# Performance work log

Hardware: AMD Instinct MI355X
Metric: run time of the kernel (lower is better)

## Reference

```python
import jax, jax.numpy as jnp
import numpy as np

S, B_BOX, C = 7, 2, 20
LAMBDA_COORD = 5.0
LAMBDA_NOOBJ = 0.5


def _iou(b1, b2):
    # b1, b2: [..., 4] in (cx, cy, w, h) format
    area1 = b1[..., 2] * b1[..., 3]
    area2 = b2[..., 2] * b2[..., 3]
    max_left = jnp.maximum(b1[..., 0] - b1[..., 2] / 2, b2[..., 0] - b2[..., 2] / 2)
    min_right = jnp.minimum(b1[..., 0] + b1[..., 2] / 2, b2[..., 0] + b2[..., 2] / 2)
    max_top = jnp.maximum(b1[..., 1] - b1[..., 3] / 2, b2[..., 1] - b2[..., 3] / 2)
    min_bottom = jnp.minimum(b1[..., 1] + b1[..., 3] / 2, b2[..., 1] + b2[..., 3] / 2)
    iw = jnp.maximum(min_right - max_left, 0.0)
    ih = jnp.maximum(min_bottom - max_top, 0.0)
    inter = iw * ih
    union = area1 + area2 - inter
    return jnp.where(inter > 0.0, inter / union, 0.0)


def setup_inputs() -> dict:
    key = jax.random.key(0)
    k1, k2, k3 = jax.random.split(key, 3)
    batch = 16384
    shape = (batch, S, S, C + 5 * B_BOX)  # [..., 30]
    pred = jax.random.uniform(k1, shape, dtype=jnp.float32)
    target = jax.random.uniform(k2, shape, dtype=jnp.float32)
    # objectness flag must be exactly 1.0 to trigger the obj branch
    obj_flag = jax.random.bernoulli(k3, 0.3, shape[:-1]).astype(jnp.float32)
    target = target.at[..., 0].set(obj_flag)
    return {"pred": pred, "target": target}


def reference(pred, target):
    batch = pred.shape[0]
    pred = pred.reshape(-1, S, S, C + 5 * B_BOX)
    target = target.reshape(-1, S, S, C + 5 * B_BOX)

    obj = (target[..., 0] == 1.0)          # [b,S,S] bool
    obj_f = obj.astype(pred.dtype)
    noobj_f = 1.0 - obj_f

    gt = target[..., 1:5]
    box1 = pred[..., 1:5]                   # predictor 1 box
    box2 = target[..., 6:10]                # NOTE: original code uses target's 2nd box
    iou1 = jax.lax.stop_gradient(_iou(box1, gt))
    iou2 = jax.lax.stop_gradient(_iou(box2, gt))
    resp1 = iou1 > iou2                     # predictor 1 responsible (strict >)
    r1 = resp1[..., None]

    # coord losses (responsible predictor)
    pxy = jnp.where(r1, pred[..., 1:3], pred[..., 6:8])
    txy = jnp.where(r1, target[..., 1:3], target[..., 6:8])
    pwh = jnp.where(r1, pred[..., 3:5], pred[..., 8:10])
    twh = jnp.where(r1, target[..., 3:5], target[..., 8:10])
    cell_xy = jnp.sum((pxy - txy) ** 2, axis=-1)
    cell_wh = jnp.sum((jnp.sqrt(pwh) - jnp.sqrt(twh)) ** 2, axis=-1)

    # obj confidence loss: responsible conf vs its iou
    conf_resp = jnp.where(resp1, pred[..., 0], pred[..., 5])
    iou_resp = jnp.where(resp1, iou1, iou2)
    cell_obj = (conf_resp - iou_resp) ** 2

    # noobj: non-responsible conf in obj cells; both confs in empty cells
    conf_other = jnp.where(resp1, pred[..., 5], pred[..., 0])
    cell_noobj_obj = conf_other ** 2
    cell_noobj_empty = pred[..., 0] ** 2 + pred[..., 5] ** 2

    cell_class = jnp.sum((pred[..., 10:] - target[..., 10:]) ** 2, axis=-1)

    loss_coord_xy = LAMBDA_COORD * jnp.sum(obj_f * cell_xy)
    loss_coord_wh = LAMBDA_COORD * jnp.sum(obj_f * cell_wh)
    loss_obj = jnp.sum(obj_f * cell_obj)
    loss_noobj = LAMBDA_NOOBJ * (jnp.sum(obj_f * cell_noobj_obj) + jnp.sum(noobj_f * cell_noobj_empty))
    loss_class = jnp.sum(obj_f * cell_class)
    loss = loss_coord_xy + loss_coord_wh + loss_obj + loss_noobj + loss_class

    bs = jnp.asarray(batch, pred.dtype)
    return ((loss_coord_xy + loss_coord_wh) / bs,
            loss_obj / bs,
            loss_noobj / bs,
            loss_class / bs,
            loss / bs)
```

## Files before the change

### kernel.cpp

```cpp
#include <hip/hip_runtime.h>

#define NCH 30
#define F2PC 15
#define CPB 256
#define THREADS 256
#define GRID 512

__device__ __forceinline__ float iou_fn(float x1, float y1, float w1, float h1,
                                        float x2, float y2, float w2, float h2) {
    float a1 = w1 * h1, a2 = w2 * h2;
    float left  = fmaxf(x1 - w1 * 0.5f, x2 - w2 * 0.5f);
    float right = fminf(x1 + w1 * 0.5f, x2 + w2 * 0.5f);
    float top   = fmaxf(y1 - h1 * 0.5f, y2 - h2 * 0.5f);
    float bot   = fminf(y1 + h1 * 0.5f, y2 + h2 * 0.5f);
    float iw = fmaxf(right - left, 0.0f);
    float ih = fmaxf(bot - top, 0.0f);
    float inter = iw * ih;
    float uni = a1 + a2 - inter;
    return (inter > 0.0f) ? (inter / uni) : 0.0f;
}

__device__ __forceinline__ void cell_losses(const float* p, const float* t,
                                            float& coord, float& lobj,
                                            float& lnoobj, float& lclass) {
    float obj_f = (t[0] == 1.0f) ? 1.0f : 0.0f;

    float iou1 = iou_fn(p[1], p[2], p[3], p[4], t[1], t[2], t[3], t[4]);
    float iou2 = iou_fn(t[6], t[7], t[8], t[9], t[1], t[2], t[3], t[4]);
    bool r = iou1 > iou2;

    float px = r ? p[1] : p[6], py = r ? p[2] : p[7];
    float pw = r ? p[3] : p[8], ph = r ? p[4] : p[9];
    float tx = r ? t[1] : t[6], ty = r ? t[2] : t[7];
    float tw = r ? t[3] : t[8], th = r ? t[4] : t[9];

    float dx = px - tx, dy = py - ty;
    float cxy = dx * dx + dy * dy;
    float swv = sqrtf(pw) - sqrtf(tw), shv = sqrtf(ph) - sqrtf(th);
    float cwh = swv * swv + shv * shv;

    float conf_resp  = r ? p[0] : p[5];
    float iou_resp   = r ? iou1 : iou2;
    float conf_other = r ? p[5] : p[0];
    float dconf = conf_resp - iou_resp;

    coord  += obj_f * (cxy + cwh);
    lobj   += obj_f * dconf * dconf;
    lnoobj += obj_f * conf_other * conf_other
            + (1.0f - obj_f) * (p[0] * p[0] + p[5] * p[5]);

    float cls = 0.0f;
#pragma unroll
    for (int i = 10; i < NCH; i++) { float e = p[i] - t[i]; cls += e * e; }
    lclass += obj_f * cls;
}

__global__ __launch_bounds__(THREADS) void yolo_main(
        const float2* __restrict__ pred2, const float2* __restrict__ targ2,
        float4* __restrict__ partials, int nchunks_full, int n_cells) {
    __shared__ float2 sp[CPB * F2PC];
    __shared__ float2 st[CPB * F2PC];

    const int tid = threadIdx.x;
    float coord = 0.f, lobj = 0.f, lnoobj = 0.f, lclass = 0.f;

    float2 rp[F2PC], rt[F2PC];

    int c = blockIdx.x;
    bool have = c < nchunks_full;
    if (have) {
        const long long b = (long long)c * (CPB * F2PC);
#pragma unroll
        for (int k = 0; k < F2PC; k++) {
            rp[k] = pred2[b + tid + k * THREADS];
            rt[k] = targ2[b + tid + k * THREADS];
        }
    }

    while (have) {
        int cn = c + gridDim.x;
        bool have_n = cn < nchunks_full;

        __syncthreads();
#pragma unroll
        for (int k = 0; k < F2PC; k++) {
            sp[tid + k * THREADS] = rp[k];
            st[tid + k * THREADS] = rt[k];
        }
        __syncthreads();

        if (have_n) {
            const long long b = (long long)cn * (CPB * F2PC);
#pragma unroll
            for (int k = 0; k < F2PC; k++) {
                rp[k] = pred2[b + tid + k * THREADS];
                rt[k] = targ2[b + tid + k * THREADS];
            }
        }

        {
            float p[NCH], t[NCH];
            const float2* pp = sp + tid * F2PC;
            const float2* tp = st + tid * F2PC;
#pragma unroll
            for (int k = 0; k < F2PC; k++) { float2 v = pp[k]; p[2 * k] = v.x; p[2 * k + 1] = v.y; }
#pragma unroll
            for (int k = 0; k < F2PC; k++) { float2 v = tp[k]; t[2 * k] = v.x; t[2 * k + 1] = v.y; }
            cell_losses(p, t, coord, lobj, lnoobj, lclass);
        }

        c = cn; have = have_n;
    }

    if (blockIdx.x == 0) {
        int cell = nchunks_full * CPB + tid;
        if (cell < n_cells) {
            float p[NCH], t[NCH];
            const float2* pp = pred2 + (long long)cell * F2PC;
            const float2* tp = targ2 + (long long)cell * F2PC;
#pragma unroll
            for (int k = 0; k < F2PC; k++) { float2 v = pp[k]; p[2 * k] = v.x; p[2 * k + 1] = v.y; }
#pragma unroll
            for (int k = 0; k < F2PC; k++) { float2 v = tp[k]; t[2 * k] = v.x; t[2 * k + 1] = v.y; }
            cell_losses(p, t, coord, lobj, lnoobj, lclass);
        }
    }

#pragma unroll
    for (int off = 32; off > 0; off >>= 1) {
        coord  += __shfl_down(coord, off);
        lobj   += __shfl_down(lobj, off);
        lnoobj += __shfl_down(lnoobj, off);
        lclass += __shfl_down(lclass, off);
    }

    __shared__ float red[4][4];
    int lane = tid & 63;
    int wid  = tid >> 6;
    if (lane == 0) {
        red[wid][0] = coord; red[wid][1] = lobj;
        red[wid][2] = lnoobj; red[wid][3] = lclass;
    }
    __syncthreads();
    if (tid == 0) {
        float s0 = 0.f, s1 = 0.f, s2 = 0.f, s3 = 0.f;
        for (int w = 0; w < 4; w++) {
            s0 += red[w][0]; s1 += red[w][1];
            s2 += red[w][2]; s3 += red[w][3];
        }
        partials[blockIdx.x] = make_float4(s0, s1, s2, s3);
    }
}

__global__ __launch_bounds__(THREADS) void yolo_reduce(
        const float4* __restrict__ partials, int nparts,
        float* __restrict__ out, double inv_bs) {
    double s0 = 0.0, s1 = 0.0, s2 = 0.0, s3 = 0.0;
    for (int i = threadIdx.x; i < nparts; i += THREADS) {
        float4 v = partials[i];
        s0 += (double)v.x; s1 += (double)v.y;
        s2 += (double)v.z; s3 += (double)v.w;
    }
#pragma unroll
    for (int off = 32; off > 0; off >>= 1) {
        s0 += __shfl_down(s0, off);
        s1 += __shfl_down(s1, off);
        s2 += __shfl_down(s2, off);
        s3 += __shfl_down(s3, off);
    }
    __shared__ double red[4][4];
    int lane = threadIdx.x & 63;
    int wid  = threadIdx.x >> 6;
    if (lane == 0) {
        red[wid][0] = s0; red[wid][1] = s1;
        red[wid][2] = s2; red[wid][3] = s3;
    }
    __syncthreads();
    if (threadIdx.x == 0) {
        double a0 = 0, a1 = 0, a2 = 0, a3 = 0;
        for (int w = 0; w < 4; w++) {
            a0 += red[w][0]; a1 += red[w][1];
            a2 += red[w][2]; a3 += red[w][3];
        }
        double cd = a0 * 5.0 * inv_bs;
        double o  = a1 * inv_bs;
        double n  = a2 * 0.5 * inv_bs;
        double cl = a3 * inv_bs;
        out[0] = (float)cd;
        out[1] = (float)o;
        out[2] = (float)n;
        out[3] = (float)cl;
        out[4] = (float)(cd + o + n + cl);
    }
}

extern "C" void kernel_launch(void* const* d_in, const int* in_sizes, int n_in,
                              void* d_out, int out_size, void* d_ws, size_t ws_size,
                              hipStream_t stream) {
    const float2* pred2 = (const float2*)d_in[0];
    const float2* targ2 = (const float2*)d_in[1];
    float* out = (float*)d_out;
    float4* partials = (float4*)d_ws;

    int n_cells = in_sizes[0] / NCH;
    int batch   = n_cells / 49;
    int nchunks_full = n_cells / CPB;
    int grid = nchunks_full < GRID ? nchunks_full : GRID;
    if (grid < 1) grid = 1;

    yolo_main<<<grid, THREADS, 0, stream>>>(pred2, targ2, partials, nchunks_full, n_cells);
    yolo_reduce<<<1, THREADS, 0, stream>>>(partials, grid, out, 1.0 / (double)batch);
}
```

Before: 210.3 us.

## Widen chunk loads to float4, stagger pred/target loads, balance grid size

Global loads for each 256-cell chunk now use 16-byte float4 accesses (7.5 per thread) in place of 15 float2 loads. The pred and target load orders are rotated against each other. The grid size is chosen so every block runs the same number of chunk iterations, which removes a partial last wave. This cuts the number of load instructions and evens out block work, at the cost of a divergent tail load for half the threads.

```diff
diff --git a/kernel.cpp b/kernel.cpp
--- a/kernel.cpp
+++ b/kernel.cpp
@@ -1,10 +1,10 @@
 #include <hip/hip_runtime.h>
 
 #define NCH 30
-#define F2PC 15
 #define CPB 256
 #define THREADS 256
-#define GRID 512
+#define F4PA 1920
+#define MAXRES 512
 
 __device__ __forceinline__ float iou_fn(float x1, float y1, float w1, float h1,
                                         float x2, float y2, float w2, float h2) {
@@ -55,27 +55,32 @@
     lclass += obj_f * cls;
 }
 
+__device__ __forceinline__ void load_chunk(const float4* __restrict__ p4,
+                                           const float4* __restrict__ t4,
+                                           long long base4, int tid,
+                                           float4* rp, float4* rt) {
+#pragma unroll
+    for (int k = 0; k < 8; k++) {
+        const int kt = (k + 4) & 7;
+        if (k < 7 || tid < 128)  rp[k]  = p4[base4 + tid + k  * THREADS];
+        if (kt < 7 || tid < 128) rt[kt] = t4[base4 + tid + kt * THREADS];
+    }
+}
+
 __global__ __launch_bounds__(THREADS) void yolo_main(
-        const float2* __restrict__ pred2, const float2* __restrict__ targ2,
+        const float4* __restrict__ pred4, const float4* __restrict__ targ4,
         float4* __restrict__ partials, int nchunks_full, int n_cells) {
-    __shared__ float2 sp[CPB * F2PC];
-    __shared__ float2 st[CPB * F2PC];
+    __shared__ float4 sp4[F4PA];
+    __shared__ float4 st4[F4PA];
 
     const int tid = threadIdx.x;
     float coord = 0.f, lobj = 0.f, lnoobj = 0.f, lclass = 0.f;
 
-    float2 rp[F2PC], rt[F2PC];
+    float4 rp[8], rt[8];
 
     int c = blockIdx.x;
     bool have = c < nchunks_full;
-    if (have) {
-        const long long b = (long long)c * (CPB * F2PC);
-#pragma unroll
-        for (int k = 0; k < F2PC; k++) {
-            rp[k] = pred2[b + tid + k * THREADS];
-            rt[k] = targ2[b + tid + k * THREADS];
-        }
-    }
+    if (have) load_chunk(pred4, targ4, (long long)c * F4PA, tid, rp, rt);
 
     while (have) {
         int cn = c + gridDim.x;
@@ -83,29 +88,25 @@
 
         __syncthreads();
 #pragma unroll
-        for (int k = 0; k < F2PC; k++) {
-            sp[tid + k * THREADS] = rp[k];
-            st[tid + k * THREADS] = rt[k];
+        for (int k = 0; k < 8; k++) {
+            if (k < 7 || tid < 128) {
+                sp4[tid + k * THREADS] = rp[k];
+                st4[tid + k * THREADS] = rt[k];
+            }
         }
         __syncthreads();
 
-        if (have_n) {
-            const long long b = (long long)cn * (CPB * F2PC);
-#pragma unroll
-            for (int k = 0; k < F2PC; k++) {
-                rp[k] = pred2[b + tid + k * THREADS];
-                rt[k] = targ2[b + tid + k * THREADS];
-            }
-        }
+        if (have_n)
+            load_chunk(pred4, targ4, (long long)cn * F4PA, tid, rp, rt);
 
         {
             float p[NCH], t[NCH];
-            const float2* pp = sp + tid * F2PC;
-            const float2* tp = st + tid * F2PC;
-#pragma unroll
-            for (int k = 0; k < F2PC; k++) { float2 v = pp[k]; p[2 * k] = v.x; p[2 * k + 1] = v.y; }
-#pragma unroll
-            for (int k = 0; k < F2PC; k++) { float2 v = tp[k]; t[2 * k] = v.x; t[2 * k + 1] = v.y; }
+            const float2* pp = reinterpret_cast<const float2*>(sp4) + tid * (NCH / 2);
+            const float2* tp = reinterpret_cast<const float2*>(st4) + tid * (NCH / 2);
+#pragma unroll
+            for (int k = 0; k < NCH / 2; k++) { float2 v = pp[k]; p[2 * k] = v.x; p[2 * k + 1] = v.y; }
+#pragma unroll
+            for (int k = 0; k < NCH / 2; k++) { float2 v = tp[k]; t[2 * k] = v.x; t[2 * k + 1] = v.y; }
             cell_losses(p, t, coord, lobj, lnoobj, lclass);
         }
 
@@ -116,12 +117,12 @@
         int cell = nchunks_full * CPB + tid;
         if (cell < n_cells) {
             float p[NCH], t[NCH];
-            const float2* pp = pred2 + (long long)cell * F2PC;
-            const float2* tp = targ2 + (long long)cell * F2PC;
-#pragma unroll
-            for (int k = 0; k < F2PC; k++) { float2 v = pp[k]; p[2 * k] = v.x; p[2 * k + 1] = v.y; }
-#pragma unroll
-            for (int k = 0; k < F2PC; k++) { float2 v = tp[k]; t[2 * k] = v.x; t[2 * k + 1] = v.y; }
+            const float2* pp = reinterpret_cast<const float2*>(pred4) + (long long)cell * (NCH / 2);
+            const float2* tp = reinterpret_cast<const float2*>(targ4) + (long long)cell * (NCH / 2);
+#pragma unroll
+            for (int k = 0; k < NCH / 2; k++) { float2 v = pp[k]; p[2 * k] = v.x; p[2 * k + 1] = v.y; }
+#pragma unroll
+            for (int k = 0; k < NCH / 2; k++) { float2 v = tp[k]; t[2 * k] = v.x; t[2 * k + 1] = v.y; }
             cell_losses(p, t, coord, lobj, lnoobj, lclass);
         }
     }
@@ -197,17 +198,23 @@
 extern "C" void kernel_launch(void* const* d_in, const int* in_sizes, int n_in,
                               void* d_out, int out_size, void* d_ws, size_t ws_size,
                               hipStream_t stream) {
-    const float2* pred2 = (const float2*)d_in[0];
-    const float2* targ2 = (const float2*)d_in[1];
+    const float4* pred4 = (const float4*)d_in[0];
+    const float4* targ4 = (const float4*)d_in[1];
     float* out = (float*)d_out;
     float4* partials = (float4*)d_ws;
 
     int n_cells = in_sizes[0] / NCH;
     int batch   = n_cells / 49;
     int nchunks_full = n_cells / CPB;
-    int grid = nchunks_full < GRID ? nchunks_full : GRID;
-    if (grid < 1) grid = 1;
-
-    yolo_main<<<grid, THREADS, 0, stream>>>(pred2, targ2, partials, nchunks_full, n_cells);
+
+    int grid;
+    if (nchunks_full <= 0) {
+        grid = 1;
+    } else {
+        int iters = (nchunks_full + MAXRES - 1) / MAXRES;
+        grid = (nchunks_full + iters - 1) / iters;
+    }
+
+    yolo_main<<<grid, THREADS, 0, stream>>>(pred4, targ4, partials, nchunks_full, n_cells);
     yolo_reduce<<<1, THREADS, 0, stream>>>(partials, grid, out, 1.0 / (double)batch);
 }
```

Result: slower. 251.2 us (+19.5%).
